# Kernel optimization log

Measured on AMD Instinct MI355X. Metric: run time of the kernel, lower is better.

## Reference

```python
import jax, jax.numpy as jnp
import numpy as np

HIDDEN = 1024
NUM_HEADS = 16
D_HEAD = HIDDEN // NUM_HEADS  # 64
SEQ = 2048
BATCH = 2


def setup_inputs() -> dict:
    key = jax.random.key(0)
    kx, kw, kb = jax.random.split(key, 3)
    x = jax.random.normal(kx, (SEQ, BATCH, HIDDEN), dtype=jnp.float32)
    W = jax.random.normal(kw, (3 * HIDDEN, HIDDEN), dtype=jnp.float32) * 0.02
    b = jax.random.normal(kb, (3 * HIDDEN,), dtype=jnp.float32) * 0.02
    return {"x": x, "W": W, "b": b}


def reference(x, W, b):
    # x: (S, B, H) seq-first, as in the torch module
    S, B, _ = x.shape
    qkv = jnp.einsum('sbh,oh->sbo', x, W) + b  # (S, B, 3*H)
    # torch views 3*hidden as (num_heads, 3, d_head): per-head-interleaved QKV
    qkv = qkv.reshape(S, B, NUM_HEADS, 3, D_HEAD)
    qkv = jnp.transpose(qkv, (2, 1, 0, 3, 4))  # (nh, B, S, 3, d)
    q, k, v = qkv[..., 0, :], qkv[..., 1, :], qkv[..., 2, :]  # each (nh, B, S, d)
    scale = 1.0 / np.sqrt(D_HEAD).astype(np.float32)
    scores = jnp.einsum('hbqd,hbkd->hbqk', q, k) * scale  # (nh, B, S, S)
    attn = jax.nn.softmax(scores, axis=-1)
    out = jnp.einsum('hbqk,hbkd->hbqd', attn, v)  # (nh, B, S, d)
    out = jnp.transpose(out, (2, 1, 0, 3)).reshape(S, B, HIDDEN)
    return out
```

## Files before the change

kernel.cpp:

```cpp
#include <hip/hip_runtime.h>
#include <hip/hip_bf16.h>


typedef __hip_bfloat16 bf16;
typedef __bf16 bfr;
typedef __attribute__((ext_vector_type(8))) __bf16 bf16x8;
typedef __attribute__((ext_vector_type(4))) __bf16 bf16x4;
typedef __attribute__((ext_vector_type(4))) float f32x4;

#define S_SEQ  2048
#define HID    1024
#define OUT3   3072
#define NROWS  4096
#define LSTR   72

#if __has_builtin(__builtin_amdgcn_exp2f)
#define EXP2F(x) __builtin_amdgcn_exp2f(x)
#else
#define EXP2F(x) exp2f(x)
#endif

#define QSCALE 0.18033688011112042f

__global__ __launch_bounds__(256) void cast_bf16_kernel(
    const float* __restrict__ src, bfr* __restrict__ dst)
{
    int gid = blockIdx.x * 256 + threadIdx.x;
    const float4* s4 = (const float4*)src;
    float4 a = s4[(size_t)gid * 2];
    float4 b = s4[(size_t)gid * 2 + 1];
    bf16x8 v;
    v[0] = (bfr)a.x; v[1] = (bfr)a.y; v[2] = (bfr)a.z; v[3] = (bfr)a.w;
    v[4] = (bfr)b.x; v[5] = (bfr)b.y; v[6] = (bfr)b.z; v[7] = (bfr)b.w;
    *(bf16x8*)(dst + (size_t)gid * 8) = v;
}

__device__ __forceinline__ void gload_lds16(const void* g, void* l) {
    __builtin_amdgcn_global_load_lds(
        (const __attribute__((address_space(1))) unsigned int*)g,
        (__attribute__((address_space(3))) unsigned int*)l, 16, 0, 0);
}

__global__ __launch_bounds__(256, 3) void qkv_gemm_mfma(
    const bfr* __restrict__ Xb, const bfr* __restrict__ Wb,
    const float* __restrict__ bias,
    bfr* __restrict__ qb, bfr* __restrict__ kb, bfr* __restrict__ vtb)
{
    __shared__ __attribute__((aligned(16))) bfr As[128 * 64];
    __shared__ __attribute__((aligned(16))) bfr Bs[128 * 64];

    const int o0 = blockIdx.x * 128;
    const int r0 = blockIdx.y * 128;
    const int tid = threadIdx.x;
    const int lane = tid & 63;
    const int w = tid >> 6;
    const int l15 = lane & 15;
    const int quad = lane >> 4;
    const int m0 = (w & 1) * 64;
    const int n0 = (w >> 1) * 64;

    f32x4 acc[4][4];
#pragma unroll
    for (int mi = 0; mi < 4; mi++)
#pragma unroll
        for (int ni = 0; ni < 4; ni++) acc[mi][ni] = {0.f, 0.f, 0.f, 0.f};

    for (int k0 = 0; k0 < HID; k0 += 64) {
#pragma unroll
        for (int i = 0; i < 4; i++) {
            int c = i * 256 + tid;
            int row = c >> 3, c8 = c & 7;
            gload_lds16(Xb + (size_t)(r0 + row) * HID + k0 + c8 * 8, As + c * 8);
            gload_lds16(Wb + (size_t)(o0 + row) * HID + k0 + c8 * 8, Bs + c * 8);
        }
        __syncthreads();

#pragma unroll
        for (int ks = 0; ks < 2; ks++) {
            bf16x8 af[4], bfg[4];
#pragma unroll
            for (int mi = 0; mi < 4; mi++)
                af[mi] = *(const bf16x8*)(As + (m0 + mi * 16 + l15) * 64 + ks * 32 + quad * 8);
#pragma unroll
            for (int ni = 0; ni < 4; ni++)
                bfg[ni] = *(const bf16x8*)(Bs + (n0 + ni * 16 + l15) * 64 + ks * 32 + quad * 8);
#pragma unroll
            for (int mi = 0; mi < 4; mi++)
#pragma unroll
                for (int ni = 0; ni < 4; ni++)
                    acc[mi][ni] = __builtin_amdgcn_mfma_f32_16x16x32_bf16(
                        af[mi], bfg[ni], acc[mi][ni], 0, 0, 0);
        }
        __syncthreads();
    }

#pragma unroll
    for (int ni = 0; ni < 4; ni++) {
        int cb = o0 + n0 + ni * 16;
        int h = cb / 192;
        int rem = cb % 192;
        int t = rem >> 6;
        int d = (rem & 63) + l15;
        float bv = bias[cb + l15];
#pragma unroll
        for (int mi = 0; mi < 4; mi++) {
#pragma unroll
            for (int r = 0; r < 4; r++) {
                int gr = r0 + m0 + mi * 16 + quad * 4 + r;
                int s = gr >> 1, b = gr & 1;
                int hb = h * 2 + b;
                float val = acc[mi][ni][r] + bv;
                if (t == 0)
                    qb[((size_t)hb * S_SEQ + s) * 64 + d] = (bfr)(val * QSCALE);
                else if (t == 1)
                    kb[((size_t)hb * S_SEQ + s) * 64 + d] = (bfr)val;
                else
                    vtb[((size_t)hb * 64 + d) * S_SEQ + s] = (bfr)val;
            }
        }
    }
}

__global__ __launch_bounds__(256, 4) void attn4_kernel(
    const bfr* __restrict__ qb, const bfr* __restrict__ kb,
    const bfr* __restrict__ vtb, float* __restrict__ out)
{
    __shared__ __attribute__((aligned(16))) bfr Ks [64 * LSTR];
    __shared__ __attribute__((aligned(16))) bfr Vts[64 * LSTR];
    __shared__ __attribute__((aligned(16))) bfr Ptq[64 * LSTR];

    const int qt = blockIdx.x;
    const int hb = blockIdx.y;
    const int h = hb >> 1, b = hb & 1;
    const int tid = threadIdx.x;
    const int lane = tid & 63;
    const int w = tid >> 6;
    const int l15 = lane & 15;
    const int quad = lane >> 4;
    const size_t hboff = (size_t)hb * S_SEQ * 64;

    const int srow0 = tid >> 3;
    const int sc8   = tid & 7;
    const int qrow = qt * 64 + 16 * w + l15;
    bf16x8 qf[2];
    qf[0] = *(const bf16x8*)(qb + hboff + (size_t)qrow * 64 + quad * 8);
    qf[1] = *(const bf16x8*)(qb + hboff + (size_t)qrow * 64 + quad * 8 + 32);

    f32x4 Oacc[4];
#pragma unroll
    for (int mt = 0; mt < 4; mt++) Oacc[mt] = {0.f, 0.f, 0.f, 0.f};
    float l_st = 0.f;

    bf16x8 kr[2], vr[2];
#pragma unroll
    for (int p = 0; p < 2; p++) {
        int row = srow0 + p * 32;
        kr[p] = *(const bf16x8*)(kb + hboff + (size_t)row * 64 + sc8 * 8);
        vr[p] = *(const bf16x8*)(vtb + hboff + (size_t)row * S_SEQ + sc8 * 8);
    }

    for (int kt = 0; kt < 32; kt++) {
        __syncthreads();
#pragma unroll
        for (int p = 0; p < 2; p++) {
            int row = srow0 + p * 32;
            *(bf16x8*)(Ks  + row * LSTR + sc8 * 8) = kr[p];
            *(bf16x8*)(Vts + row * LSTR + sc8 * 8) = vr[p];
        }
        {
            int ktn = kt + 1 < 32 ? kt + 1 : 31;
#pragma unroll
            for (int p = 0; p < 2; p++) {
                int row = srow0 + p * 32;
                kr[p] = *(const bf16x8*)(kb + hboff + (size_t)(ktn * 64 + row) * 64 + sc8 * 8);
                vr[p] = *(const bf16x8*)(vtb + hboff + (size_t)row * S_SEQ + ktn * 64 + sc8 * 8);
            }
        }
        __syncthreads();

        f32x4 sc[4];
#pragma unroll
        for (int mt = 0; mt < 4; mt++) sc[mt] = {0.f, 0.f, 0.f, 0.f};
#pragma unroll
        for (int k0 = 0; k0 < 2; k0++) {
#pragma unroll
            for (int mt = 0; mt < 4; mt++) {
                bf16x8 kf = *(const bf16x8*)(Ks + (mt * 16 + l15) * LSTR + quad * 8 + 32 * k0);
                sc[mt] = __builtin_amdgcn_mfma_f32_16x16x32_bf16(kf, qf[k0], sc[mt], 0, 0, 0);
            }
        }

        float rs = 0.f;
#pragma unroll
        for (int mt = 0; mt < 4; mt++) {
            bf16x4 pk;
#pragma unroll
            for (int r = 0; r < 4; r++) {
                float pv = EXP2F(sc[mt][r]);
                rs += pv;
                pk[r] = (bfr)pv;
            }
            *(bf16x4*)(Ptq + (16 * w + l15) * LSTR + mt * 16 + quad * 4) = pk;
        }
        rs += __shfl_xor(rs, 16);
        rs += __shfl_xor(rs, 32);
        l_st += rs;

#pragma unroll
        for (int k0 = 0; k0 < 2; k0++) {
            bf16x8 pf = *(const bf16x8*)(Ptq + (16 * w + l15) * LSTR + quad * 8 + 32 * k0);
#pragma unroll
            for (int mt = 0; mt < 4; mt++) {
                bf16x8 vf = *(const bf16x8*)(Vts + (mt * 16 + l15) * LSTR + quad * 8 + 32 * k0);
                Oacc[mt] = __builtin_amdgcn_mfma_f32_16x16x32_bf16(vf, pf, Oacc[mt], 0, 0, 0);
            }
        }
    }

    float inv = 1.0f / l_st;
    float* orow = out + ((size_t)qrow * 2 + b) * HID + h * 64;
#pragma unroll
    for (int mt = 0; mt < 4; mt++) {
        float4 o4;
        o4.x = Oacc[mt][0] * inv;
        o4.y = Oacc[mt][1] * inv;
        o4.z = Oacc[mt][2] * inv;
        o4.w = Oacc[mt][3] * inv;
        *(float4*)(orow + mt * 16 + quad * 4) = o4;
    }
}

extern "C" void kernel_launch(void* const* d_in, const int* in_sizes, int n_in,
                              void* d_out, int out_size, void* d_ws, size_t ws_size,
                              hipStream_t stream) {
    const float* X    = (const float*)d_in[0];
    const float* W    = (const float*)d_in[1];
    const float* bias = (const float*)d_in[2];
    float* out = (float*)d_out;

    bfr* qb  = (bfr*)d_ws;
    bfr* kb  = qb + (size_t)32 * S_SEQ * 64;
    bfr* vtb = kb + (size_t)32 * S_SEQ * 64;

    bfr* Xb = (bfr*)d_out;
    bfr* Wb = Xb + (size_t)NROWS * HID;

    cast_bf16_kernel<<<NROWS * HID / (256 * 8), 256, 0, stream>>>(X, Xb);
    cast_bf16_kernel<<<OUT3 * HID / (256 * 8), 256, 0, stream>>>(W, Wb);

    dim3 g1(OUT3 / 128, NROWS / 128);
    qkv_gemm_mfma<<<g1, 256, 0, stream>>>(Xb, Wb, bias, qb, kb, vtb);

    dim3 g2(S_SEQ / 64, 32);
    attn4_kernel<<<g2, 256, 0, stream>>>(qb, kb, vtb, out);
}
```

Measured before the change: 179.4 us.

## Split attention keys across waves with LDS reduction and merge cast kernels

The attention kernel now gives each block 32 queries and hands every wave its own quarter of the key range. Each wave reads K and V straight from global memory instead of staging them through shared LDS tiles, which removes the per-tile barriers. Partial outputs and row sums are then combined through LDS at the end. The two fp32-to-bf16 cast launches are merged into one to save a launch. The cost is redundant global K/V reads across query tiles (twice as many tiles), a larger final reduction, and more registers per wave.

Result: slower. 235.9 us (+31.5%).

```diff
diff --git a/kernel.cpp b/kernel.cpp
--- a/kernel.cpp
+++ b/kernel.cpp
@@ -12,7 +12,7 @@
 #define HID    1024
 #define OUT3   3072
 #define NROWS  4096
-#define LSTR   72
+#define PSTR   72
 
 #if __has_builtin(__builtin_amdgcn_exp2f)
 #define EXP2F(x) __builtin_amdgcn_exp2f(x)
@@ -22,10 +22,17 @@
 
 #define QSCALE 0.18033688011112042f
 
-__global__ __launch_bounds__(256) void cast_bf16_kernel(
-    const float* __restrict__ src, bfr* __restrict__ dst)
+__global__ __launch_bounds__(256) void cast_both_kernel(
+    const float* __restrict__ X, bfr* __restrict__ Xb,
+    const float* __restrict__ W, bfr* __restrict__ Wb)
 {
-    int gid = blockIdx.x * 256 + threadIdx.x;
+    int bid = blockIdx.x;
+    const float* src;
+    bfr* dst;
+    int lid;
+    if (bid < NROWS * HID / 2048) { src = X; dst = Xb; lid = bid; }
+    else { src = W; dst = Wb; lid = bid - NROWS * HID / 2048; }
+    int gid = lid * 256 + threadIdx.x;
     const float4* s4 = (const float4*)src;
     float4 a = s4[(size_t)gid * 2];
     float4 b = s4[(size_t)gid * 2 + 1];
@@ -121,13 +128,12 @@
     }
 }
 
-__global__ __launch_bounds__(256, 4) void attn4_kernel(
+__global__ __launch_bounds__(256, 4) void attn5_kernel(
     const bfr* __restrict__ qb, const bfr* __restrict__ kb,
     const bfr* __restrict__ vtb, float* __restrict__ out)
 {
-    __shared__ __attribute__((aligned(16))) bfr Ks [64 * LSTR];
-    __shared__ __attribute__((aligned(16))) bfr Vts[64 * LSTR];
-    __shared__ __attribute__((aligned(16))) bfr Ptq[64 * LSTR];
+    __shared__ __attribute__((aligned(16))) unsigned char lds_raw[4 * 64 * 33 * 4];
+    __shared__ float Lp[4][32];
 
     const int qt = blockIdx.x;
     const int hb = blockIdx.y;
@@ -139,94 +145,114 @@
     const int quad = lane >> 4;
     const size_t hboff = (size_t)hb * S_SEQ * 64;
 
-    const int srow0 = tid >> 3;
-    const int sc8   = tid & 7;
-    const int qrow = qt * 64 + 16 * w + l15;
-    bf16x8 qf[2];
-    qf[0] = *(const bf16x8*)(qb + hboff + (size_t)qrow * 64 + quad * 8);
-    qf[1] = *(const bf16x8*)(qb + hboff + (size_t)qrow * 64 + quad * 8 + 32);
-
-    f32x4 Oacc[4];
-#pragma unroll
-    for (int mt = 0; mt < 4; mt++) Oacc[mt] = {0.f, 0.f, 0.f, 0.f};
-    float l_st = 0.f;
-
-    bf16x8 kr[2], vr[2];
-#pragma unroll
-    for (int p = 0; p < 2; p++) {
-        int row = srow0 + p * 32;
-        kr[p] = *(const bf16x8*)(kb + hboff + (size_t)row * 64 + sc8 * 8);
-        vr[p] = *(const bf16x8*)(vtb + hboff + (size_t)row * S_SEQ + sc8 * 8);
-    }
-
-    for (int kt = 0; kt < 32; kt++) {
-        __syncthreads();
-#pragma unroll
-        for (int p = 0; p < 2; p++) {
-            int row = srow0 + p * 32;
-            *(bf16x8*)(Ks  + row * LSTR + sc8 * 8) = kr[p];
-            *(bf16x8*)(Vts + row * LSTR + sc8 * 8) = vr[p];
-        }
-        {
-            int ktn = kt + 1 < 32 ? kt + 1 : 31;
-#pragma unroll
-            for (int p = 0; p < 2; p++) {
-                int row = srow0 + p * 32;
-                kr[p] = *(const bf16x8*)(kb + hboff + (size_t)(ktn * 64 + row) * 64 + sc8 * 8);
-                vr[p] = *(const bf16x8*)(vtb + hboff + (size_t)row * S_SEQ + ktn * 64 + sc8 * 8);
+    bfr* Ptq = (bfr*)lds_raw + (size_t)w * 32 * PSTR;
+    float* Osum = (float*)lds_raw;
+
+    bf16x8 qf[2][2];
+#pragma unroll
+    for (int nt = 0; nt < 2; nt++)
+#pragma unroll
+        for (int ks = 0; ks < 2; ks++)
+            qf[nt][ks] = *(const bf16x8*)(qb + hboff +
+                (size_t)(qt * 32 + nt * 16 + l15) * 64 + quad * 8 + 32 * ks);
+
+    f32x4 O[4][2];
+#pragma unroll
+    for (int mt = 0; mt < 4; mt++)
+#pragma unroll
+        for (int nt = 0; nt < 2; nt++) O[mt][nt] = {0.f, 0.f, 0.f, 0.f};
+    float lsum[2] = {0.f, 0.f};
+
+    for (int kt = 0; kt < 8; kt++) {
+        const int kb0 = w * 512 + kt * 64;
+
+        f32x4 sc[4][2];
+#pragma unroll
+        for (int mt = 0; mt < 4; mt++)
+#pragma unroll
+            for (int nt = 0; nt < 2; nt++) sc[mt][nt] = {0.f, 0.f, 0.f, 0.f};
+#pragma unroll
+        for (int ks = 0; ks < 2; ks++) {
+            bf16x8 kf[4];
+#pragma unroll
+            for (int mt = 0; mt < 4; mt++)
+                kf[mt] = *(const bf16x8*)(kb + hboff +
+                    (size_t)(kb0 + mt * 16 + l15) * 64 + quad * 8 + 32 * ks);
+#pragma unroll
+            for (int mt = 0; mt < 4; mt++)
+#pragma unroll
+                for (int nt = 0; nt < 2; nt++)
+                    sc[mt][nt] = __builtin_amdgcn_mfma_f32_16x16x32_bf16(
+                        kf[mt], qf[nt][ks], sc[mt][nt], 0, 0, 0);
+        }
+
+#pragma unroll
+        for (int nt = 0; nt < 2; nt++) {
+#pragma unroll
+            for (int mt = 0; mt < 4; mt++) {
+                bf16x4 pk;
+#pragma unroll
+                for (int r = 0; r < 4; r++) {
+                    float pv = EXP2F(sc[mt][nt][r]);
+                    lsum[nt] += pv;
+                    pk[r] = (bfr)pv;
+                }
+                *(bf16x4*)(Ptq + (nt * 16 + l15) * PSTR + mt * 16 + quad * 4) = pk;
             }
         }
-        __syncthreads();
-
-        f32x4 sc[4];
-#pragma unroll
-        for (int mt = 0; mt < 4; mt++) sc[mt] = {0.f, 0.f, 0.f, 0.f};
-#pragma unroll
-        for (int k0 = 0; k0 < 2; k0++) {
-#pragma unroll
-            for (int mt = 0; mt < 4; mt++) {
-                bf16x8 kf = *(const bf16x8*)(Ks + (mt * 16 + l15) * LSTR + quad * 8 + 32 * k0);
-                sc[mt] = __builtin_amdgcn_mfma_f32_16x16x32_bf16(kf, qf[k0], sc[mt], 0, 0, 0);
-            }
-        }
-
-        float rs = 0.f;
-#pragma unroll
-        for (int mt = 0; mt < 4; mt++) {
-            bf16x4 pk;
-#pragma unroll
-            for (int r = 0; r < 4; r++) {
-                float pv = EXP2F(sc[mt][r]);
-                rs += pv;
-                pk[r] = (bfr)pv;
-            }
-            *(bf16x4*)(Ptq + (16 * w + l15) * LSTR + mt * 16 + quad * 4) = pk;
-        }
-        rs += __shfl_xor(rs, 16);
-        rs += __shfl_xor(rs, 32);
-        l_st += rs;
-
-#pragma unroll
-        for (int k0 = 0; k0 < 2; k0++) {
-            bf16x8 pf = *(const bf16x8*)(Ptq + (16 * w + l15) * LSTR + quad * 8 + 32 * k0);
-#pragma unroll
-            for (int mt = 0; mt < 4; mt++) {
-                bf16x8 vf = *(const bf16x8*)(Vts + (mt * 16 + l15) * LSTR + quad * 8 + 32 * k0);
-                Oacc[mt] = __builtin_amdgcn_mfma_f32_16x16x32_bf16(vf, pf, Oacc[mt], 0, 0, 0);
-            }
-        }
-    }
-
-    float inv = 1.0f / l_st;
-    float* orow = out + ((size_t)qrow * 2 + b) * HID + h * 64;
-#pragma unroll
-    for (int mt = 0; mt < 4; mt++) {
-        float4 o4;
-        o4.x = Oacc[mt][0] * inv;
-        o4.y = Oacc[mt][1] * inv;
-        o4.z = Oacc[mt][2] * inv;
-        o4.w = Oacc[mt][3] * inv;
-        *(float4*)(orow + mt * 16 + quad * 4) = o4;
+
+#pragma unroll
+        for (int ks = 0; ks < 2; ks++) {
+            bf16x8 vf[4], pf[2];
+#pragma unroll
+            for (int mt = 0; mt < 4; mt++)
+                vf[mt] = *(const bf16x8*)(vtb + hboff +
+                    (size_t)(mt * 16 + l15) * S_SEQ + kb0 + quad * 8 + 32 * ks);
+#pragma unroll
+            for (int nt = 0; nt < 2; nt++)
+                pf[nt] = *(const bf16x8*)(Ptq + (nt * 16 + l15) * PSTR + quad * 8 + 32 * ks);
+#pragma unroll
+            for (int mt = 0; mt < 4; mt++)
+#pragma unroll
+                for (int nt = 0; nt < 2; nt++)
+                    O[mt][nt] = __builtin_amdgcn_mfma_f32_16x16x32_bf16(
+                        vf[mt], pf[nt], O[mt][nt], 0, 0, 0);
+        }
+    }
+
+#pragma unroll
+    for (int nt = 0; nt < 2; nt++) {
+        lsum[nt] += __shfl_xor(lsum[nt], 16);
+        lsum[nt] += __shfl_xor(lsum[nt], 32);
+    }
+    if (quad == 0) { Lp[w][l15] = lsum[0]; Lp[w][16 + l15] = lsum[1]; }
+
+    __syncthreads();
+
+#pragma unroll
+    for (int mt = 0; mt < 4; mt++)
+#pragma unroll
+        for (int nt = 0; nt < 2; nt++)
+#pragma unroll
+            for (int r = 0; r < 4; r++)
+                Osum[((size_t)w * 64 + mt * 16 + quad * 4 + r) * 33 + nt * 16 + l15]
+                    = O[mt][nt][r];
+
+    __syncthreads();
+
+    {
+        const int d = w * 16 + l15;
+#pragma unroll
+        for (int i = 0; i < 8; i++) {
+            int q = quad + 4 * i;
+            float acc = 0.f;
+#pragma unroll
+            for (int wv = 0; wv < 4; wv++)
+                acc += Osum[((size_t)wv * 64 + d) * 33 + q];
+            float lt = Lp[0][q] + Lp[1][q] + Lp[2][q] + Lp[3][q];
+            int s = qt * 32 + q;
+            out[((size_t)s * 2 + b) * HID + h * 64 + d] = acc / lt;
+        }
     }
 }
 
@@ -245,12 +271,11 @@
     bfr* Xb = (bfr*)d_out;
     bfr* Wb = Xb + (size_t)NROWS * HID;
 
-    cast_bf16_kernel<<<NROWS * HID / (256 * 8), 256, 0, stream>>>(X, Xb);
-    cast_bf16_kernel<<<OUT3 * HID / (256 * 8), 256, 0, stream>>>(W, Wb);
+    cast_both_kernel<<<(NROWS * HID + OUT3 * HID) / 2048, 256, 0, stream>>>(X, Xb, W, Wb);
 
     dim3 g1(OUT3 / 128, NROWS / 128);
     qkv_gemm_mfma<<<g1, 256, 0, stream>>>(Xb, Wb, bias, qb, kb, vtb);
 
-    dim3 g2(S_SEQ / 64, 32);
-    attn4_kernel<<<g2, 256, 0, stream>>>(qb, kb, vtb, out);
-}
+    dim3 g2(S_SEQ / 32, 32);
+    attn5_kernel<<<g2, 256, 0, stream>>>(qb, kb, vtb, out);
+}
```
